# Kernel tuning notes

Measured on AMD Instinct MI355X. Metric: run time of the kernel, lower is better.

The kernel has to match this reference:

```python
import jax, jax.numpy as jnp
import numpy as np

N, D, T = 4096, 512, 4096
TEMPERATURE = 0.07
MARGIN = 0.5
CONT_WEIGHT = 1.0
TRIP_WEIGHT = 0.3
EPS = 1e-8        # eps in the log / denominator (matches torch code)
PD_EPS = 1e-6     # F.pairwise_distance default eps added to the difference


def setup_inputs() -> dict:
    key = jax.random.key(0)
    k1, k2, k3 = jax.random.split(key, 3)
    embeddings = jax.random.normal(k1, (N, D), dtype=jnp.float32)
    labels = jax.random.randint(k2, (N,), 0, 256)            # ~16 positives per place
    triplets = jax.random.randint(k3, (T, 3), 0, N)          # (anchor, pos, neg) indices
    return {"embeddings": embeddings, "labels": labels, "triplets": triplets}


def reference(embeddings, labels, triplets):
    # ---- MultiPositiveContrastiveLoss ----
    # F.cosine_similarity normalizes each row with eps=1e-8 on the norm.
    norms = jnp.linalg.norm(embeddings, axis=1, keepdims=True)
    n_emb = embeddings / jnp.maximum(norms, EPS)
    sim = (n_emb @ n_emb.T) / TEMPERATURE                    # [N, N]

    pos_mask = (labels[:, None] == labels[None, :]).astype(embeddings.dtype)
    pos_mask = pos_mask * (1.0 - jnp.eye(sim.shape[0], dtype=embeddings.dtype))

    exp_sim = jnp.exp(sim)
    pos_sum = (exp_sim * pos_mask).sum(axis=1)
    total_sum = exp_sim.sum(axis=1)
    loss = -jnp.log(pos_sum / (total_sum + EPS) + EPS)

    valid = pos_mask.sum(axis=1) > 0
    cnt = valid.sum()
    cont_loss = jnp.where(
        cnt > 0,
        jnp.where(valid, loss, 0.0).sum() / jnp.maximum(cnt, 1).astype(loss.dtype),
        jnp.zeros((), loss.dtype),
    )

    # ---- TripletLoss, vectorized over all triplets (replaces Python loop) ----
    a = embeddings[triplets[:, 0]]   # [T, D]
    p = embeddings[triplets[:, 1]]
    ng = embeddings[triplets[:, 2]]
    pos_dist = jnp.linalg.norm(a - p + PD_EPS, axis=1)
    neg_dist = jnp.linalg.norm(a - ng + PD_EPS, axis=1)
    trip_loss = jnp.maximum(pos_dist - neg_dist + MARGIN, 0.0).mean()

    total = CONT_WEIGHT * cont_loss + TRIP_WEIGHT * trip_loss
    return (total, cont_loss, trip_loss)
```

## Files before the change

### kernel.cpp

```cpp
#include <hip/hip_runtime.h>

#define NN 4096
#define DD 512
#define TT 4096

typedef __bf16 bf16x8 __attribute__((ext_vector_type(8)));
typedef float f32x4 __attribute__((ext_vector_type(4)));

constexpr float INV_TEMP = 1.0f / 0.07f;

#define AS1(p) ((__attribute__((address_space(1))) const void*)(p))
#define AS3(p) ((__attribute__((address_space(3))) void*)(p))

__global__ __launch_bounds__(256) void k_normtrip(const float* __restrict__ emb,
                                                  __bf16* __restrict__ nemb,
                                                  const int* __restrict__ trip,
                                                  float* __restrict__ tl) {
    int wave = threadIdx.x >> 6, lane = threadIdx.x & 63;
    int row = blockIdx.x * 4 + wave;

    int ia = trip[row * 3 + 0], ip = trip[row * 3 + 1], ig = trip[row * 3 + 2];
    const float4* pa = (const float4*)(emb + (size_t)ia * DD);
    const float4* pp = (const float4*)(emb + (size_t)ip * DD);
    const float4* pn = (const float4*)(emb + (size_t)ig * DD);
    float d1 = 0.0f, d2 = 0.0f;
    #pragma unroll
    for (int j = 0; j < 2; ++j) {
        float4 a = pa[lane * 2 + j];
        float4 p = pp[lane * 2 + j];
        float4 n = pn[lane * 2 + j];
        float dx;
        dx = a.x - p.x + 1e-6f; d1 += dx * dx;
        dx = a.y - p.y + 1e-6f; d1 += dx * dx;
        dx = a.z - p.z + 1e-6f; d1 += dx * dx;
        dx = a.w - p.w + 1e-6f; d1 += dx * dx;
        dx = a.x - n.x + 1e-6f; d2 += dx * dx;
        dx = a.y - n.y + 1e-6f; d2 += dx * dx;
        dx = a.z - n.z + 1e-6f; d2 += dx * dx;
        dx = a.w - n.w + 1e-6f; d2 += dx * dx;
    }

    const float4* src = (const float4*)(emb + (size_t)row * DD);
    float4 x0 = src[lane * 2 + 0];
    float4 x1 = src[lane * 2 + 1];
    float ss = x0.x * x0.x + x0.y * x0.y + x0.z * x0.z + x0.w * x0.w +
               x1.x * x1.x + x1.y * x1.y + x1.z * x1.z + x1.w * x1.w;
    #pragma unroll
    for (int m = 1; m < 64; m <<= 1) ss += __shfl_xor(ss, m, 64);
    float inv = 1.0f / fmaxf(sqrtf(ss), 1e-8f);
    bf16x8 v;
    v[0] = (__bf16)(x0.x * inv); v[1] = (__bf16)(x0.y * inv);
    v[2] = (__bf16)(x0.z * inv); v[3] = (__bf16)(x0.w * inv);
    v[4] = (__bf16)(x1.x * inv); v[5] = (__bf16)(x1.y * inv);
    v[6] = (__bf16)(x1.z * inv); v[7] = (__bf16)(x1.w * inv);
    *(bf16x8*)(nemb + (size_t)row * DD + lane * 8) = v;

    #pragma unroll
    for (int m = 1; m < 64; m <<= 1) {
        d1 += __shfl_xor(d1, m, 64);
        d2 += __shfl_xor(d2, m, 64);
    }
    if (lane == 0) tl[row] = fmaxf(sqrtf(d1) - sqrtf(d2) + 0.5f, 0.0f);
}


__global__ __launch_bounds__(512, 2) void k_contrast(const __bf16* __restrict__ nemb,
                                                     const int* __restrict__ labels,
                                                     float* __restrict__ posP,
                                                     float* __restrict__ totP) {
    __shared__ __attribute__((aligned(16))) __bf16 aS[2][256 * 64];
    __shared__ __attribute__((aligned(16))) __bf16 bS[2][256 * 64];
    __shared__ int rlab[256];
    __shared__ int clab[256];

    int tid = threadIdx.x;
    int lane = tid & 63, wave = tid >> 6;
    int wr = wave >> 2, wc = wave & 3;
    int l15 = lane & 15, quad = lane >> 4;
    int swz = l15 & 7;

    int bid = blockIdx.x;
    int xcd = bid & 7, idx = bid >> 3;
    int rowblk = (xcd >> 1) * 4 + (idx >> 3);
    int colblk = (xcd & 1) * 8 + (idx & 7);
    int row0 = rowblk * 256, col0 = colblk * 256;

    if (tid < 256) rlab[tid] = labels[row0 + tid];
    else           clab[tid - 256] = labels[col0 + tid - 256];

    int srr = (tid >> 3) & 7;
    int scol = ((tid & 7) ^ srr) * 8;
    const __bf16* gA0 = nemb + (size_t)(row0 + wave * 32 + srr) * DD + scol;
    const __bf16* gB0 = nemb + (size_t)(col0 + wave * 32 + srr) * DD + scol;
    int ldst = wave * 2048 + (tid & 63) * 8;

    f32x4 acc[8][4];
    #pragma unroll
    for (int fm = 0; fm < 8; ++fm)
        #pragma unroll
        for (int fn = 0; fn < 4; ++fn) {
            f32x4 z = {0.0f, 0.0f, 0.0f, 0.0f};
            acc[fm][fn] = z;
        }

    #pragma unroll
    for (int j = 0; j < 4; ++j) {
        __builtin_amdgcn_global_load_lds(AS1(gA0 + (size_t)(j * 8) * DD),
                                         AS3(&aS[0][ldst + j * 512]), 16, 0, 0);
        __builtin_amdgcn_global_load_lds(AS1(gB0 + (size_t)(j * 8) * DD),
                                         AS3(&bS[0][ldst + j * 512]), 16, 0, 0);
    }
    __syncthreads();

    #pragma unroll
    for (int kt = 0; kt < 8; ++kt) {
        int cur = kt & 1;
        if (kt < 7) {
            #pragma unroll
            for (int j = 0; j < 4; ++j) {
                __builtin_amdgcn_global_load_lds(AS1(gA0 + (size_t)(j * 8) * DD + (kt + 1) * 64),
                                                 AS3(&aS[cur ^ 1][ldst + j * 512]), 16, 0, 0);
                __builtin_amdgcn_global_load_lds(AS1(gB0 + (size_t)(j * 8) * DD + (kt + 1) * 64),
                                                 AS3(&bS[cur ^ 1][ldst + j * 512]), 16, 0, 0);
            }
        }
        #pragma unroll
        for (int kc = 0; kc < 2; ++kc) {
            bf16x8 af[8], bf[4];
            #pragma unroll
            for (int fm = 0; fm < 8; ++fm)
                af[fm] = *(const bf16x8*)(&aS[cur][(wr * 128 + fm * 16 + l15) * 64 +
                                                   (((kc * 4 + quad) ^ swz) * 8)]);
            #pragma unroll
            for (int fn = 0; fn < 4; ++fn)
                bf[fn] = *(const bf16x8*)(&bS[cur][(wc * 64 + fn * 16 + l15) * 64 +
                                                   (((kc * 4 + quad) ^ swz) * 8)]);
            #pragma unroll
            for (int fm = 0; fm < 8; ++fm)
                #pragma unroll
                for (int fn = 0; fn < 4; ++fn)
                    acc[fm][fn] = __builtin_amdgcn_mfma_f32_16x16x32_bf16(
                        af[fm], bf[fn], acc[fm][fn], 0, 0, 0);
        }
        __syncthreads();
    }

    #pragma unroll
    for (int fm = 0; fm < 8; ++fm) {
        int rloc = wr * 128 + fm * 16 + quad * 4;
        int gibase = row0 + rloc;
        int rl[4];
        #pragma unroll
        for (int v = 0; v < 4; ++v) rl[v] = rlab[rloc + v];
        float tv[4] = {0, 0, 0, 0}, pv[4] = {0, 0, 0, 0};
        #pragma unroll
        for (int fn = 0; fn < 4; ++fn) {
            int cloc = wc * 64 + fn * 16 + l15;
            int cl = clab[cloc];
            int gj = col0 + cloc;
            f32x4 a = acc[fm][fn];
            #pragma unroll
            for (int v = 0; v < 4; ++v) {
                float e = __expf(a[v] * INV_TEMP);
                tv[v] += e;
                bool match = (rl[v] == cl) && ((gibase + v) != gj);
                pv[v] += match ? e : 0.0f;
            }
        }
        #pragma unroll
        for (int m = 1; m < 16; m <<= 1) {
            #pragma unroll
            for (int v = 0; v < 4; ++v) {
                tv[v] += __shfl_xor(tv[v], m, 64);
                pv[v] += __shfl_xor(pv[v], m, 64);
            }
        }
        if (l15 == 0) {
            #pragma unroll
            for (int v = 0; v < 4; ++v) {
                int o = (gibase + v) * 64 + colblk * 4 + wc;
                posP[o] = pv[v];
                totP[o] = tv[v];
            }
        }
    }
}

__global__ __launch_bounds__(256) void k_rowloss(const float* __restrict__ posP,
                                                 const float* __restrict__ totP,
                                                 const int* __restrict__ labels,
                                                 float* __restrict__ rloss,
                                                 float* __restrict__ rvalid) {
    __shared__ int hist[256];
    int tid = threadIdx.x;
    hist[tid] = 0;
    __syncthreads();
    #pragma unroll
    for (int j = 0; j < 16; ++j)
        atomicAdd(&hist[labels[tid + j * 256]], 1);
    __syncthreads();

    int wave = tid >> 6, lane = tid & 63;
    int row = blockIdx.x * 4 + wave;
    float p = posP[row * 64 + lane];
    float t = totP[row * 64 + lane];
    #pragma unroll
    for (int m = 1; m < 64; m <<= 1) {
        p += __shfl_xor(p, m, 64);
        t += __shfl_xor(t, m, 64);
    }
    if (lane == 0) {
        bool valid = hist[labels[row]] > 1;
        float loss = valid ? -logf(p / (t + 1e-8f) + 1e-8f) : 0.0f;
        rloss[row] = loss;
        rvalid[row] = valid ? 1.0f : 0.0f;
    }
}

__global__ __launch_bounds__(256) void k_final(const float* __restrict__ rloss,
                                               const float* __restrict__ rvalid,
                                               const float* __restrict__ tl,
                                               float* __restrict__ out) {
    int tid = threadIdx.x;
    float sl = 0.0f, sv = 0.0f, st = 0.0f;
    for (int i = tid; i < NN; i += 256) {
        sl += rloss[i];
        sv += rvalid[i];
        st += tl[i];
    }
    #pragma unroll
    for (int m = 1; m < 64; m <<= 1) {
        sl += __shfl_xor(sl, m, 64);
        sv += __shfl_xor(sv, m, 64);
        st += __shfl_xor(st, m, 64);
    }
    __shared__ float red[3][4];
    int lane = tid & 63, wave = tid >> 6;
    if (lane == 0) { red[0][wave] = sl; red[1][wave] = sv; red[2][wave] = st; }
    __syncthreads();
    if (tid == 0) {
        float SL = red[0][0] + red[0][1] + red[0][2] + red[0][3];
        float SV = red[1][0] + red[1][1] + red[1][2] + red[1][3];
        float ST = red[2][0] + red[2][1] + red[2][2] + red[2][3];
        float cont = (SV > 0.0f) ? (SL / SV) : 0.0f;
        float trip = ST * (1.0f / (float)TT);
        out[0] = cont + 0.3f * trip;
        out[1] = cont;
        out[2] = trip;
    }
}

extern "C" void kernel_launch(void* const* d_in, const int* in_sizes, int n_in,
                              void* d_out, int out_size, void* d_ws, size_t ws_size,
                              hipStream_t stream) {
    const float* emb = (const float*)d_in[0];
    const int* labels = (const int*)d_in[1];
    const int* trips = (const int*)d_in[2];
    float* out = (float*)d_out;
    char* ws = (char*)d_ws;

    __bf16* nemb  = (__bf16*)(ws);
    float* posP   = (float*)(ws + 4194304);
    float* totP   = (float*)(ws + 5242880);
    float* rloss  = (float*)(ws + 6291456);
    float* rvalid = (float*)(ws + 6307840);
    float* tl     = (float*)(ws + 6324224);

    k_normtrip<<<NN / 4, 256, 0, stream>>>(emb, nemb, trips, tl);
    k_contrast<<<256, 512, 0, stream>>>(nemb, labels, posP, totP);
    k_rowloss<<<NN / 4, 256, 0, stream>>>(posP, totP, labels, rloss, rvalid);
    k_final<<<1, 256, 0, stream>>>(rloss, rvalid, tl, out);
}
```

Baseline: 103.7 us.

## Exploit similarity symmetry: compute only upper-triangle tiles and emit column partials

The contrastive kernel now tiles the N×N similarity matrix into 128×128 blocks and launches only the upper-triangular tiles (528 blocks instead of 256 full-grid 256×256 tiles). Each off-diagonal tile also accumulates column-wise sums of exp and positive-masked exp, writing them as the mirrored row partials. This roughly halves the GEMM and exp work. In exchange it uses smaller tiles with less operand reuse, a serial while-loop to map block id to tile, extra shuffles, and a mapping of blocks to XCDs that is no longer tuned.

```diff
diff --git a/kernel.cpp b/kernel.cpp
--- a/kernel.cpp
+++ b/kernel.cpp
@@ -64,29 +64,29 @@
 }
 
 
-__global__ __launch_bounds__(512, 2) void k_contrast(const __bf16* __restrict__ nemb,
+__global__ __launch_bounds__(256, 2) void k_contrast(const __bf16* __restrict__ nemb,
                                                      const int* __restrict__ labels,
                                                      float* __restrict__ posP,
                                                      float* __restrict__ totP) {
-    __shared__ __attribute__((aligned(16))) __bf16 aS[2][256 * 64];
-    __shared__ __attribute__((aligned(16))) __bf16 bS[2][256 * 64];
-    __shared__ int rlab[256];
-    __shared__ int clab[256];
+    __shared__ __attribute__((aligned(16))) __bf16 aS[2][128 * 64];
+    __shared__ __attribute__((aligned(16))) __bf16 bS[2][128 * 64];
+    __shared__ int rlab[128];
+    __shared__ int clab[128];
 
     int tid = threadIdx.x;
     int lane = tid & 63, wave = tid >> 6;
-    int wr = wave >> 2, wc = wave & 3;
+    int wr = wave >> 1, wc = wave & 1;
     int l15 = lane & 15, quad = lane >> 4;
     int swz = l15 & 7;
 
-    int bid = blockIdx.x;
-    int xcd = bid & 7, idx = bid >> 3;
-    int rowblk = (xcd >> 1) * 4 + (idx >> 3);
-    int colblk = (xcd & 1) * 8 + (idx & 7);
-    int row0 = rowblk * 256, col0 = colblk * 256;
-
-    if (tid < 256) rlab[tid] = labels[row0 + tid];
-    else           clab[tid - 256] = labels[col0 + tid - 256];
+    int t = (blockIdx.x & 7) * 66 + (blockIdx.x >> 3);
+    int r = 0;
+    while (t >= 32 - r) { t -= 32 - r; ++r; }
+    int c = r + t;
+    int row0 = r * 128, col0 = c * 128;
+
+    if (tid < 128) rlab[tid] = labels[row0 + tid];
+    else if (tid < 256) clab[tid - 128] = labels[col0 + tid - 128];
 
     int srr = (tid >> 3) & 7;
     int scol = ((tid & 7) ^ srr) * 8;
@@ -94,9 +94,9 @@
     const __bf16* gB0 = nemb + (size_t)(col0 + wave * 32 + srr) * DD + scol;
     int ldst = wave * 2048 + (tid & 63) * 8;
 
-    f32x4 acc[8][4];
-    #pragma unroll
-    for (int fm = 0; fm < 8; ++fm)
+    f32x4 acc[4][4];
+    #pragma unroll
+    for (int fm = 0; fm < 4; ++fm)
         #pragma unroll
         for (int fn = 0; fn < 4; ++fn) {
             f32x4 z = {0.0f, 0.0f, 0.0f, 0.0f};
@@ -126,17 +126,17 @@
         }
         #pragma unroll
         for (int kc = 0; kc < 2; ++kc) {
-            bf16x8 af[8], bf[4];
-            #pragma unroll
-            for (int fm = 0; fm < 8; ++fm)
-                af[fm] = *(const bf16x8*)(&aS[cur][(wr * 128 + fm * 16 + l15) * 64 +
+            bf16x8 af[4], bf[4];
+            #pragma unroll
+            for (int fm = 0; fm < 4; ++fm)
+                af[fm] = *(const bf16x8*)(&aS[cur][(wr * 64 + fm * 16 + l15) * 64 +
                                                    (((kc * 4 + quad) ^ swz) * 8)]);
             #pragma unroll
             for (int fn = 0; fn < 4; ++fn)
                 bf[fn] = *(const bf16x8*)(&bS[cur][(wc * 64 + fn * 16 + l15) * 64 +
                                                    (((kc * 4 + quad) ^ swz) * 8)]);
             #pragma unroll
-            for (int fm = 0; fm < 8; ++fm)
+            for (int fm = 0; fm < 4; ++fm)
                 #pragma unroll
                 for (int fn = 0; fn < 4; ++fn)
                     acc[fm][fn] = __builtin_amdgcn_mfma_f32_16x16x32_bf16(
@@ -145,9 +145,10 @@
         __syncthreads();
     }
 
-    #pragma unroll
-    for (int fm = 0; fm < 8; ++fm) {
-        int rloc = wr * 128 + fm * 16 + quad * 4;
+    float tc[4] = {0, 0, 0, 0}, pc[4] = {0, 0, 0, 0};
+    #pragma unroll
+    for (int fm = 0; fm < 4; ++fm) {
+        int rloc = wr * 64 + fm * 16 + quad * 4;
         int gibase = row0 + rloc;
         int rl[4];
         #pragma unroll
@@ -164,7 +165,10 @@
                 float e = __expf(a[v] * INV_TEMP);
                 tv[v] += e;
                 bool match = (rl[v] == cl) && ((gibase + v) != gj);
-                pv[v] += match ? e : 0.0f;
+                float pe = match ? e : 0.0f;
+                pv[v] += pe;
+                tc[fn] += e;
+                pc[fn] += pe;
             }
         }
         #pragma unroll
@@ -178,9 +182,28 @@
         if (l15 == 0) {
             #pragma unroll
             for (int v = 0; v < 4; ++v) {
-                int o = (gibase + v) * 64 + colblk * 4 + wc;
+                int o = (gibase + v) * 64 + c * 2 + wc;
                 posP[o] = pv[v];
                 totP[o] = tv[v];
+            }
+        }
+    }
+
+    if (r != c) {
+        #pragma unroll
+        for (int fn = 0; fn < 4; ++fn) {
+            tc[fn] += __shfl_xor(tc[fn], 16, 64);
+            tc[fn] += __shfl_xor(tc[fn], 32, 64);
+            pc[fn] += __shfl_xor(pc[fn], 16, 64);
+            pc[fn] += __shfl_xor(pc[fn], 32, 64);
+        }
+        if (quad == 0) {
+            #pragma unroll
+            for (int fn = 0; fn < 4; ++fn) {
+                int gcol = col0 + wc * 64 + fn * 16 + l15;
+                int o = gcol * 64 + r * 2 + wr;
+                posP[o] = pc[fn];
+                totP[o] = tc[fn];
             }
         }
     }
@@ -267,7 +290,7 @@
     float* tl     = (float*)(ws + 6324224);
 
     k_normtrip<<<NN / 4, 256, 0, stream>>>(emb, nemb, trips, tl);
-    k_contrast<<<256, 512, 0, stream>>>(nemb, labels, posP, totP);
+    k_contrast<<<528, 256, 0, stream>>>(nemb, labels, posP, totP);
     k_rowloss<<<NN / 4, 256, 0, stream>>>(posP, totP, labels, rloss, rvalid);
     k_final<<<1, 256, 0, stream>>>(rloss, rvalid, tl, out);
 }
```

New measurement: 101.2 us. 1.02x faster.
